# Kernel optimization log

Hardware: AMD Instinct MI355X
Metric: run time of the kernel (lower is better)

## Reference

```python
import jax, jax.numpy as jnp
import numpy as np

N, D = 8192, 128
NOISEVAR = 1.0

def _softplusinverse(v):
    return np.log(1.0 - np.exp(-v)) + v

def setup_inputs() -> dict:
    key = jax.random.key(0)
    kx, kn = jax.random.split(key)
    x = jax.random.normal(kx, (N, D), dtype=jnp.float32)
    noise = jax.random.normal(kn, (N, D), dtype=jnp.float32)
    phi = jnp.asarray(_softplusinverse(NOISEVAR), dtype=jnp.float32)
    return {"x": x, "phi": phi, "noise": noise}

def reference(x, phi, noise):
    # x: [n, d] encoded features; phi: scalar noise param; noise: [n, d] i.i.d. N(0,1)
    n = x.shape[0]
    var = jax.nn.softplus(phi)
    # Pairwise squared L2 distances via Gram-matrix trick (same math as
    # norm(x_i - x_j)^2, avoids the [n, n, d] broadcast intermediate).
    sq = jnp.sum(x * x, axis=1)                                  # [n]
    d2 = jnp.maximum(sq[:, None] + sq[None, :] - 2.0 * (x @ x.T), 0.0)  # [n, n]
    kde_contribution = jnp.mean(jax.nn.logsumexp(-0.5 * d2 / var, axis=1))
    IXT_nats = jnp.log(jnp.float32(n)) - kde_contribution
    IXT = IXT_nats / jnp.log(jnp.float32(2.0))  # bits=True -> nats2bits
    out = x + var * noise                        # training=True noise injection
    return out, IXT
```

## Files before the change

### kernel.cpp

```cpp
#include <hip/hip_runtime.h>
#include <hip/hip_bf16.h>

#define N 8192
#define D 128
#define T64 64
#define NT64 (N / T64)

typedef __attribute__((ext_vector_type(4))) int intx4;
typedef unsigned long long u64;

static __device__ inline float softplus_of(const float* __restrict__ phi) {
    float p = phi[0];
    return (p > 20.f) ? p : log1pf(__expf(p));
}

__global__ __launch_bounds__(256) void k1_prep(
        const float* __restrict__ x, const float* __restrict__ phi,
        const float* __restrict__ noise, float* __restrict__ out,
        signed char* __restrict__ q8, int* __restrict__ sqv,
        float* __restrict__ rowsum) {
    int gid = blockIdx.x * 256 + threadIdx.x;
    int row = gid >> 4;
    int gc  = gid & 15;
    float var = softplus_of(phi);

    const float* xs = x     + (size_t)row * D + gc * 8;
    const float* ns = noise + (size_t)row * D + gc * 8;
    float4 u  = *(const float4*)xs, v  = *(const float4*)(xs + 4);
    float4 nu = *(const float4*)ns, nv = *(const float4*)(ns + 4);

    float4 o0, o1;
    o0.x = u.x + var * nu.x; o0.y = u.y + var * nu.y;
    o0.z = u.z + var * nu.z; o0.w = u.w + var * nu.w;
    o1.x = v.x + var * nv.x; o1.y = v.y + var * nv.y;
    o1.z = v.z + var * nv.z; o1.w = v.w + var * nv.w;
    float* od = out + (size_t)row * D + gc * 8;
    *(float4*)od = o0; *(float4*)(od + 4) = o1;

    float f[8] = {u.x, u.y, u.z, u.w, v.x, v.y, v.z, v.w};
    u64 pack = 0;
    int s = 0;
    #pragma unroll
    for (int k = 0; k < 8; k++) {
        float c = fminf(fmaxf(f[k] * 16.f, -127.f), 127.f);
        int q = (int)rintf(c);
        s += q * q;
        pack |= ((u64)(q & 255)) << (8 * k);
    }
    *(u64*)&q8[(size_t)row * D + gc * 8] = pack;

    #pragma unroll
    for (int m = 1; m < 16; m <<= 1) s += __shfl_xor(s, m, 64);
    if (gc == 0) { sqv[row] = s; rowsum[row] = 0.f; }
}

__global__ __launch_bounds__(256, 3) void k2_gram(
        const signed char* __restrict__ q8, const float* __restrict__ phi,
        const int* __restrict__ sqv, float* __restrict__ rowsum) {
    const int w    = blockIdx.x * 4 + (threadIdx.x >> 6);
    const int lane = threadIdx.x & 63;
    const int lrow = lane & 15;
    const int quad = lane >> 4;

    const int cnt = (w < 2112) ? 3 : 2;
    int start     = (w < 2112) ? 3 * w : 2 * w + 2112;
    int ti = 0, rem = start, len = NT64;
    while (rem >= len) { rem -= len; ++ti; --len; }
    int tj = ti + rem;

    float var = softplus_of(phi);
    const float c2 = ((-0.5f / var) * 1.4426950408889634f) * (1.f / 256.f);
    const int Ts = (int)ceilf(30.f / (-c2));

    intx4 af[4][2], bf[4][2];
    int   sqi[4][4];
    int curTi = -1;

    #pragma unroll
    for (int nt = 0; nt < 4; nt++) {
        const signed char* br = q8 + (size_t)(tj * T64 + nt * 16 + lrow) * D + quad * 16;
        bf[nt][0] = *(const intx4*)br;
        bf[nt][1] = *(const intx4*)(br + 64);
    }

    for (int r = 0; r < cnt; ++r) {
        const int iB = ti * T64, jB = tj * T64;

        int sje[4];
        #pragma unroll
        for (int nt = 0; nt < 4; nt++)
            sje[nt] = sqv[jB + nt * 16 + lrow];

        if (ti != curTi) {
            #pragma unroll
            for (int mt = 0; mt < 4; mt++) {
                const signed char* ar =
                    q8 + (size_t)(iB + mt * 16 + lrow) * D + quad * 16;
                af[mt][0] = *(const intx4*)ar;
                af[mt][1] = *(const intx4*)(ar + 64);
            }
            #pragma unroll
            for (int mt = 0; mt < 4; mt++)
                #pragma unroll
                for (int reg = 0; reg < 4; reg++)
                    sqi[mt][reg] = sqv[iB + mt * 16 + quad * 4 + reg];
            curTi = ti;
        }

        int nti = ti, ntj = tj + 1;
        if (ntj == NT64) { ++nti; ntj = nti; }
        const bool more = (r + 1 < cnt);

        #pragma unroll
        for (int nt = 0; nt < 4; nt++) {
            intx4 acc[4] = {};
            #pragma unroll
            for (int kk = 0; kk < 2; kk++)
                #pragma unroll
                for (int mt = 0; mt < 4; mt++)
                    acc[mt] = __builtin_amdgcn_mfma_i32_16x16x64_i8(
                        af[mt][kk], bf[nt][kk], acc[mt], 0, 0, 0);

            if (more) {
                const signed char* br =
                    q8 + (size_t)(ntj * T64 + nt * 16 + lrow) * D + quad * 16;
                bf[nt][0] = *(const intx4*)br;
                bf[nt][1] = *(const intx4*)(br + 64);
            }

            const int sj = sje[nt];
            int mn = 0x7fffffff;
            #pragma unroll
            for (int mt = 0; mt < 4; mt++)
                #pragma unroll
                for (int reg = 0; reg < 4; reg++) {
                    int d2s = sqi[mt][reg] + sj - (acc[mt][reg] << 1);
                    mn = min(mn, d2s);
                }

            if (__any(mn < Ts)) {
                float colv = 0.f;
                #pragma unroll
                for (int mt = 0; mt < 4; mt++)
                    #pragma unroll
                    for (int reg = 0; reg < 4; reg++) {
                        int d2s = sqi[mt][reg] + sj - (acc[mt][reg] << 1);
                        float p = __builtin_amdgcn_exp2f((float)d2s * c2);
                        colv += p;
                        float rv = p;
                        rv += __shfl_xor(rv, 1, 64);
                        rv += __shfl_xor(rv, 2, 64);
                        rv += __shfl_xor(rv, 4, 64);
                        rv += __shfl_xor(rv, 8, 64);
                        if (lrow == 0)
                            atomicAdd(&rowsum[iB + mt * 16 + quad * 4 + reg], rv);
                    }
                if (ti != tj) {
                    colv += __shfl_xor(colv, 16, 64);
                    colv += __shfl_xor(colv, 32, 64);
                    if (quad == 0)
                        atomicAdd(&rowsum[jB + nt * 16 + lrow], colv);
                }
            }
        }

        ti = nti; tj = ntj;
    }
}

__global__ __launch_bounds__(1024) void k3_final(
        const float* __restrict__ rowsum, float* __restrict__ out_ixt) {
    __shared__ float red[16];
    int t = threadIdx.x;
    float local = 0.f;
    for (int i = t; i < N; i += 1024) local += logf(rowsum[i]);
    #pragma unroll
    for (int m = 1; m < 64; m <<= 1) local += __shfl_xor(local, m, 64);
    if ((t & 63) == 0) red[t >> 6] = local;
    __syncthreads();
    if (t < 16) {
        float v = red[t];
        #pragma unroll
        for (int m = 1; m < 16; m <<= 1) v += __shfl_xor(v, m, 64);
        if (t == 0) {
            float kde = v / (float)N;
            out_ixt[0] = (logf((float)N) - kde) * 1.4426950408889634f;
        }
    }
}

extern "C" void kernel_launch(void* const* d_in, const int* in_sizes, int n_in,
                              void* d_out, int out_size, void* d_ws, size_t ws_size,
                              hipStream_t stream) {
    const float* x     = (const float*)d_in[0];
    const float* phi   = (const float*)d_in[1];
    const float* noise = (const float*)d_in[2];
    float* out = (float*)d_out;

    float* rowsum = (float*)d_ws;
    int*   sqv    = (int*)(rowsum + N);
    signed char* q8 = (signed char*)(sqv + N);

    k1_prep<<<(N * 16) / 256, 256, 0, stream>>>(x, phi, noise, out, q8, sqv, rowsum);
    k2_gram<<<768, 256, 0, stream>>>(q8, phi, sqv, rowsum);
    k3_final<<<1, 1024, 0, stream>>>(rowsum, out + (size_t)N * D);
}
```

Baseline: 92.25 us.

## Fuse noise output and final reduction into gram kernel with norm-bound skip

The noise-injection output moves from the prep kernel into the gram kernel, and the separate final-reduction kernel is removed in favour of a last-block-done pattern driven by an atomic counter. The skip test for a tile becomes a bound on the largest Gram entry against the global minimum row norm, which is gathered by atomicMin in the prep kernel. Row norms are now loaded only inside tiles that pass the test. The grid grows to 1024 blocks so each block also stores one float4 of output. The gain comes from one fewer launch and fewer norm loads. The risk is that ctrl[1] is never reset to a large value before atomicMin, so skipping depends on the workspace's prior contents, and the looser bound may let more tiles through to the exp path.

```diff
diff --git a/kernel.cpp b/kernel.cpp
--- a/kernel.cpp
+++ b/kernel.cpp
@@ -5,38 +5,28 @@
 #define D 128
 #define T64 64
 #define NT64 (N / T64)
+#define GRID_KB 1024
 
 typedef __attribute__((ext_vector_type(4))) int intx4;
 typedef unsigned long long u64;
+typedef unsigned int u32;
 
 static __device__ inline float softplus_of(const float* __restrict__ phi) {
     float p = phi[0];
     return (p > 20.f) ? p : log1pf(__expf(p));
 }
 
-__global__ __launch_bounds__(256) void k1_prep(
-        const float* __restrict__ x, const float* __restrict__ phi,
-        const float* __restrict__ noise, float* __restrict__ out,
-        signed char* __restrict__ q8, int* __restrict__ sqv,
-        float* __restrict__ rowsum) {
+
+__global__ __launch_bounds__(256) void kA_prep(
+        const float* __restrict__ x, signed char* __restrict__ q8,
+        int* __restrict__ sqv, float* __restrict__ rowsum,
+        u32* __restrict__ ctrl) {
     int gid = blockIdx.x * 256 + threadIdx.x;
     int row = gid >> 4;
     int gc  = gid & 15;
-    float var = softplus_of(phi);
-
-    const float* xs = x     + (size_t)row * D + gc * 8;
-    const float* ns = noise + (size_t)row * D + gc * 8;
-    float4 u  = *(const float4*)xs, v  = *(const float4*)(xs + 4);
-    float4 nu = *(const float4*)ns, nv = *(const float4*)(ns + 4);
-
-    float4 o0, o1;
-    o0.x = u.x + var * nu.x; o0.y = u.y + var * nu.y;
-    o0.z = u.z + var * nu.z; o0.w = u.w + var * nu.w;
-    o1.x = v.x + var * nv.x; o1.y = v.y + var * nv.y;
-    o1.z = v.z + var * nv.z; o1.w = v.w + var * nv.w;
-    float* od = out + (size_t)row * D + gc * 8;
-    *(float4*)od = o0; *(float4*)(od + 4) = o1;
-
+
+    const float* xs = x + (size_t)row * D + gc * 8;
+    float4 u = *(const float4*)xs, v = *(const float4*)(xs + 4);
     float f[8] = {u.x, u.y, u.z, u.w, v.x, v.y, v.z, v.w};
     u64 pack = 0;
     int s = 0;
@@ -52,28 +42,41 @@
     #pragma unroll
     for (int m = 1; m < 16; m <<= 1) s += __shfl_xor(s, m, 64);
     if (gc == 0) { sqv[row] = s; rowsum[row] = 0.f; }
-}
-
-__global__ __launch_bounds__(256, 3) void k2_gram(
-        const signed char* __restrict__ q8, const float* __restrict__ phi,
-        const int* __restrict__ sqv, float* __restrict__ rowsum) {
-    const int w    = blockIdx.x * 4 + (threadIdx.x >> 6);
-    const int lane = threadIdx.x & 63;
+
+    u32 ms = (u32)s;
+    ms = min(ms, (u32)__shfl_xor((int)ms, 16, 64));
+    ms = min(ms, (u32)__shfl_xor((int)ms, 32, 64));
+    if ((threadIdx.x & 63) == 0) atomicMin(&ctrl[1], ms);
+    if (gid == 0) ctrl[0] = 0;
+}
+
+__global__ __launch_bounds__(256, 3) void kB_gram(
+        const float* __restrict__ x, const float* __restrict__ phi,
+        const float* __restrict__ noise, float* __restrict__ out,
+        const signed char* __restrict__ q8, const int* __restrict__ sqv,
+        float* __restrict__ rowsum, u32* __restrict__ ctrl) {
+    const int tid  = threadIdx.x;
+    const int w    = blockIdx.x * 4 + (tid >> 6);
+    const int lane = tid & 63;
     const int lrow = lane & 15;
     const int quad = lane >> 4;
 
-    const int cnt = (w < 2112) ? 3 : 2;
-    int start     = (w < 2112) ? 3 * w : 2 * w + 2112;
+    const int og = blockIdx.x * 256 + tid;
+    float4 xv = ((const float4*)x)[og];
+    float4 nv = ((const float4*)noise)[og];
+
+    float var = softplus_of(phi);
+    const float c2 = ((-0.5f / var) * 1.4426950408889634f) * (1.f / 256.f);
+    const int  Ts = (int)ceilf(30.f / (-c2));
+    const int  thr2 = 2 * (int)ctrl[1] - Ts;
+
+    const int cnt = (w < 64) ? 3 : 2;
+    int start     = (w < 64) ? 3 * w : 2 * w + 64;
     int ti = 0, rem = start, len = NT64;
     while (rem >= len) { rem -= len; ++ti; --len; }
     int tj = ti + rem;
 
-    float var = softplus_of(phi);
-    const float c2 = ((-0.5f / var) * 1.4426950408889634f) * (1.f / 256.f);
-    const int Ts = (int)ceilf(30.f / (-c2));
-
     intx4 af[4][2], bf[4][2];
-    int   sqi[4][4];
     int curTi = -1;
 
     #pragma unroll
@@ -86,24 +89,13 @@
     for (int r = 0; r < cnt; ++r) {
         const int iB = ti * T64, jB = tj * T64;
 
-        int sje[4];
-        #pragma unroll
-        for (int nt = 0; nt < 4; nt++)
-            sje[nt] = sqv[jB + nt * 16 + lrow];
-
         if (ti != curTi) {
             #pragma unroll
             for (int mt = 0; mt < 4; mt++) {
-                const signed char* ar =
-                    q8 + (size_t)(iB + mt * 16 + lrow) * D + quad * 16;
+                const signed char* ar = q8 + (size_t)(iB + mt * 16 + lrow) * D + quad * 16;
                 af[mt][0] = *(const intx4*)ar;
                 af[mt][1] = *(const intx4*)(ar + 64);
             }
-            #pragma unroll
-            for (int mt = 0; mt < 4; mt++)
-                #pragma unroll
-                for (int reg = 0; reg < 4; reg++)
-                    sqi[mt][reg] = sqv[iB + mt * 16 + quad * 4 + reg];
             curTi = ti;
         }
 
@@ -128,23 +120,22 @@
                 bf[nt][1] = *(const intx4*)(br + 64);
             }
 
-            const int sj = sje[nt];
-            int mn = 0x7fffffff;
+            int lm = acc[0][0];
             #pragma unroll
             for (int mt = 0; mt < 4; mt++)
                 #pragma unroll
-                for (int reg = 0; reg < 4; reg++) {
-                    int d2s = sqi[mt][reg] + sj - (acc[mt][reg] << 1);
-                    mn = min(mn, d2s);
-                }
-
-            if (__any(mn < Ts)) {
+                for (int reg = 0; reg < 4; reg++)
+                    lm = max(lm, acc[mt][reg]);
+
+            if (__any(2 * lm > thr2)) {
+                const int sj = sqv[jB + nt * 16 + lrow];
                 float colv = 0.f;
                 #pragma unroll
                 for (int mt = 0; mt < 4; mt++)
                     #pragma unroll
                     for (int reg = 0; reg < 4; reg++) {
-                        int d2s = sqi[mt][reg] + sj - (acc[mt][reg] << 1);
+                        int si = sqv[iB + mt * 16 + quad * 4 + reg];
+                        int d2s = si + sj - (acc[mt][reg] << 1);
                         float p = __builtin_amdgcn_exp2f((float)d2s * c2);
                         colv += p;
                         float rv = p;
@@ -166,25 +157,31 @@
 
         ti = nti; tj = ntj;
     }
-}
-
-__global__ __launch_bounds__(1024) void k3_final(
-        const float* __restrict__ rowsum, float* __restrict__ out_ixt) {
-    __shared__ float red[16];
-    int t = threadIdx.x;
-    float local = 0.f;
-    for (int i = t; i < N; i += 1024) local += logf(rowsum[i]);
-    #pragma unroll
-    for (int m = 1; m < 64; m <<= 1) local += __shfl_xor(local, m, 64);
-    if ((t & 63) == 0) red[t >> 6] = local;
+
+    float4 ov;
+    ov.x = xv.x + var * nv.x; ov.y = xv.y + var * nv.y;
+    ov.z = xv.z + var * nv.z; ov.w = xv.w + var * nv.w;
+    ((float4*)out)[og] = ov;
+
+    __shared__ int amLast;
+    __shared__ float red[4];
     __syncthreads();
-    if (t < 16) {
-        float v = red[t];
+    if (tid == 0) {
+        __threadfence();
+        amLast = (atomicAdd(&ctrl[0], 1u) == GRID_KB - 1);
+    }
+    __syncthreads();
+    if (amLast) {
+        __threadfence();
+        float local = 0.f;
+        for (int i = tid; i < N; i += 256) local += logf(rowsum[i]);
         #pragma unroll
-        for (int m = 1; m < 16; m <<= 1) v += __shfl_xor(v, m, 64);
-        if (t == 0) {
-            float kde = v / (float)N;
-            out_ixt[0] = (logf((float)N) - kde) * 1.4426950408889634f;
+        for (int m = 1; m < 64; m <<= 1) local += __shfl_xor(local, m, 64);
+        if ((tid & 63) == 0) red[tid >> 6] = local;
+        __syncthreads();
+        if (tid == 0) {
+            float kde = (red[0] + red[1] + red[2] + red[3]) / (float)N;
+            out[(size_t)N * D] = (logf((float)N) - kde) * 1.4426950408889634f;
         }
     }
 }
@@ -197,11 +194,11 @@
     const float* noise = (const float*)d_in[2];
     float* out = (float*)d_out;
 
-    float* rowsum = (float*)d_ws;
+    u32*   ctrl   = (u32*)d_ws;
+    float* rowsum = (float*)((char*)d_ws + 256);
     int*   sqv    = (int*)(rowsum + N);
     signed char* q8 = (signed char*)(sqv + N);
 
-    k1_prep<<<(N * 16) / 256, 256, 0, stream>>>(x, phi, noise, out, q8, sqv, rowsum);
-    k2_gram<<<768, 256, 0, stream>>>(q8, phi, sqv, rowsum);
-    k3_final<<<1, 1024, 0, stream>>>(rowsum, out + (size_t)N * D);
-}
+    kA_prep<<<(N * 16) / 256, 256, 0, stream>>>(x, q8, sqv, rowsum, ctrl);
+    kB_gram<<<GRID_KB, 256, 0, stream>>>(x, phi, noise, out, q8, sqv, rowsum, ctrl);
+}
```

After: 156.5 us. +69.7%, slower.
